# Kernel tuning notes

Measured on AMD Instinct MI355X. Metric: run time of the kernel, lower is better.

Reference implementation:

```python
import jax, jax.numpy as jnp
import numpy as np

N_NODES = 100000


def gcn_conv(x, edge_src, edge_dst, edge_weight, W, b):
    # support = x @ W ; out = A @ support + b  (A given as weighted edge list)
    h = x @ W                                   # [N, d_out]
    msg = h[edge_src] * edge_weight[:, None]     # [E, d_out]
    agg = jax.ops.segment_sum(msg, edge_dst, num_segments=N_NODES)
    return agg + b


def setup_inputs() -> dict:
    key = jax.random.key(0)
    ks = jax.random.split(key, 8)
    N, E, m, hidden, m_y = N_NODES, 1600000, 128, 64, 32
    x = jax.random.normal(ks[0], (N, m), dtype=jnp.float32)
    edge_src = jax.random.randint(ks[1], (E,), 0, N, dtype=jnp.int32)
    edge_dst = jax.random.randint(ks[2], (E,), 0, N, dtype=jnp.int32)
    edge_weight = jax.random.uniform(ks[3], (E,), dtype=jnp.float32)
    s1 = 1.0 / np.sqrt(m)
    s2 = 1.0 / np.sqrt(hidden)
    W1 = jax.random.uniform(ks[4], (m, hidden), dtype=jnp.float32, minval=-s1, maxval=s1)
    b1 = jax.random.uniform(ks[5], (hidden,), dtype=jnp.float32, minval=-s1, maxval=s1)
    W2 = jax.random.uniform(ks[6], (hidden, m_y), dtype=jnp.float32, minval=-s2, maxval=s2)
    b2 = jax.random.uniform(ks[7], (m_y,), dtype=jnp.float32, minval=-s2, maxval=s2)
    return {"x": x, "edge_src": edge_src, "edge_dst": edge_dst,
            "edge_weight": edge_weight, "W1": W1, "b1": b1, "W2": W2, "b2": b2}


def reference(x, edge_src, edge_dst, edge_weight, W1, b1, W2, b2):
    out = gcn_conv(x, edge_src, edge_dst, edge_weight, W1, b1)
    out = jax.nn.relu(out)
    # F.dropout(p=0.5, training=self.training) -> identity in eval mode
    out = gcn_conv(out, edge_src, edge_dst, edge_weight, W2, b2)
    return out
```

## Files before the change

### kernel.cpp

```cpp
#include <hip/hip_runtime.h>
#include <hip/hip_bf16.h>


typedef unsigned short u16;
typedef unsigned int uint;
typedef short short8 __attribute__((ext_vector_type(8)));
typedef float floatx4 __attribute__((ext_vector_type(4)));

static __device__ __forceinline__ u16 f2bf(float f) {
    unsigned int u = __float_as_uint(f);
    return (u16)((u + 0x7fff + ((u >> 16) & 1)) >> 16);
}

#define F4C(v, j) ((j)==0?(v).x:((j)==1?(v).y:((j)==2?(v).z:(v).w)))
#define CHUNK 2048

__global__ __launch_bounds__(256) void init_kernel(
    const float* __restrict__ W1, u16* __restrict__ wfg, int* __restrict__ gcursor)
{
    const int idx = blockIdx.x * 256 + threadIdx.x;
    if (idx < 512) gcursor[idx] = 0;
    const float4 v = ((const float4*)W1)[idx];
    const int k = idx >> 4, n4 = (idx & 15) * 4;
    const int step = k >> 5, klane = (k >> 3) & 3, j = k & 7;
    #pragma unroll
    for (int c = 0; c < 4; c++) {
        int n = n4 + c;
        wfg[(((n >> 4) * 4 + step) * 64 + klane * 16 + (n & 15)) * 8 + j] = f2bf(F4C(v, c));
    }
}

union __align__(16) SharedU {
    struct {
        u16 xs[64][136];
        u16 wf[4][4][64][8];
    } g;
    struct {
        int2 stage[CHUNK];
        u16  stb[CHUNK];
        int  hist[512], sc[512], xscan[512], place[512], runbase[512];
    } p;
};

__global__ __launch_bounds__(256, 4) void g1p_kernel(
    const float* __restrict__ x, const u16* __restrict__ wfg,
    u16* __restrict__ h1, int N,
    const int* __restrict__ src, const int* __restrict__ dst,
    const float* __restrict__ w, int* __restrict__ gcursor,
    int2* __restrict__ es, int E, int cap, int pblocks)
{
    __shared__ SharedU sh;
    const int tid = threadIdx.x;

    if (blockIdx.x < pblocks) {
        const int base = blockIdx.x * CHUNK;
        const int nloc = min(CHUNK, E - base);

        sh.p.hist[tid] = 0; sh.p.hist[tid + 256] = 0;
        __syncthreads();
        for (int i = tid; i < nloc; i += 256)
            atomicAdd(&sh.p.hist[dst[base + i] >> 8], 1);
        __syncthreads();

        sh.p.sc[tid] = sh.p.hist[tid];
        sh.p.sc[tid + 256] = sh.p.hist[tid + 256];
        __syncthreads();
        for (int o = 1; o < 512; o <<= 1) {
            int v0 = (tid >= o) ? sh.p.sc[tid - o] : 0;
            int v1 = (tid + 256 >= o) ? sh.p.sc[tid + 256 - o] : 0;
            __syncthreads();
            sh.p.sc[tid] += v0;
            sh.p.sc[tid + 256] += v1;
            __syncthreads();
        }
        sh.p.xscan[tid] = sh.p.sc[tid] - sh.p.hist[tid];
        sh.p.xscan[tid + 256] = sh.p.sc[tid + 256] - sh.p.hist[tid + 256];
        sh.p.place[tid] = sh.p.xscan[tid];
        sh.p.place[tid + 256] = sh.p.xscan[tid + 256];
        __syncthreads();

        for (int i = tid; i < nloc; i += 256) {
            int d = dst[base + i];
            int b = d >> 8;
            int pos = atomicAdd(&sh.p.place[b], 1);
            sh.p.stage[pos] = make_int2(src[base + i] | ((d & 255) << 24),
                                        __float_as_int(w[base + i]));
            sh.p.stb[pos] = (u16)b;
        }
        __syncthreads();

        {
            int l0 = sh.p.hist[tid], l1 = sh.p.hist[tid + 256];
            sh.p.runbase[tid]       = l0 ? atomicAdd(&gcursor[tid], l0)       : 0;
            sh.p.runbase[tid + 256] = l1 ? atomicAdd(&gcursor[tid + 256], l1) : 0;
        }
        __syncthreads();

        for (int i = tid; i < nloc; i += 256) {
            int b = sh.p.stb[i];
            es[(size_t)b * cap + sh.p.runbase[b] + (i - sh.p.xscan[b])] = sh.p.stage[i];
        }
        return;
    }

    const int row0 = (blockIdx.x - pblocks) * 64;
    {
        const float4* wg4 = (const float4*)wfg;
        float4* wl4 = (float4*)&sh.g.wf[0][0][0][0];
        #pragma unroll
        for (int i = 0; i < 4; i++) wl4[tid + i*256] = wg4[tid + i*256];
    }
    {
        const float4* x4 = (const float4*)x;
        #pragma unroll
        for (int i = 0; i < 8; i++) {
            int idx = tid + i*256;
            int r = idx >> 5, kc = idx & 31;
            int gr = row0 + r;
            float4 v = make_float4(0.f,0.f,0.f,0.f);
            if (gr < N) v = x4[gr*32 + kc];
            ushort4 o;
            o.x = f2bf(v.x); o.y = f2bf(v.y); o.z = f2bf(v.z); o.w = f2bf(v.w);
            *(ushort4*)&sh.g.xs[r][kc*4] = o;
        }
    }
    __syncthreads();

    const int wave = tid >> 6, lane = tid & 63;
    const int m = lane & 15, quad = lane >> 4;
    const int rw = wave * 16;

    floatx4 acc[4] = {(floatx4)(0.f), (floatx4)(0.f), (floatx4)(0.f), (floatx4)(0.f)};
    #pragma unroll
    for (int step = 0; step < 4; step++) {
        short8 a = *(const short8*)&sh.g.xs[rw + m][step*32 + quad*8];
        #pragma unroll
        for (int nt = 0; nt < 4; nt++) {
            short8 b = *(const short8*)&sh.g.wf[nt][step][lane][0];
            acc[nt] = __builtin_amdgcn_mfma_f32_16x16x32_bf16(a, b, acc[nt], 0, 0, 0);
        }
    }
    #pragma unroll
    for (int nt = 0; nt < 4; nt++) {
        #pragma unroll
        for (int r = 0; r < 4; r++) {
            int gr = row0 + rw + quad*4 + r;
            if (gr < N) h1[(size_t)gr*64 + nt*16 + m] = f2bf(acc[nt][r]);
        }
    }
}

#define SCAP 6144
__global__ __launch_bounds__(512, 3) void sort2_kernel(
    const int2* __restrict__ es, const int* __restrict__ gcursor,
    int2* __restrict__ es2, int2* __restrict__ off2, int N, int cap, int nb)
{
    __shared__ int2 stage[SCAP];
    __shared__ int hist[256], sc[256], cur[256];
    const int t = threadIdx.x;
    const int b = blockIdx.x;
    const int e0 = b * cap;
    const int len = gcursor[b];
    const int nstage = min(len, SCAP);

    if (t < 256) hist[t] = 0;
    __syncthreads();
    for (int i = t; i < nstage; i += 512) {
        int2 e = es[e0 + i];
        stage[i] = e;
        atomicAdd(&hist[((unsigned)e.x) >> 24], 1);
    }
    for (int i = SCAP + t; i < len; i += 512)
        atomicAdd(&hist[((unsigned)es[e0 + i].x) >> 24], 1);
    __syncthreads();

    int v = 0;
    if (t < 256) { v = hist[t]; sc[t] = v; }
    __syncthreads();
    for (int o = 1; o < 256; o <<= 1) {
        int add = 0;
        if (t < 256 && t >= o) add = sc[t - o];
        __syncthreads();
        if (t < 256) sc[t] += add;
        __syncthreads();
    }
    if (t < 256) {
        int ex = sc[t] - v;
        cur[t] = ex;
        int g = b * 256 + t;
        if (g < N) off2[g] = make_int2(e0 + ex, e0 + ex + v);
    }
    __syncthreads();

    for (int i = t; i < nstage; i += 512) {
        int2 e = stage[i];
        int pos = e0 + atomicAdd(&cur[((unsigned)e.x) >> 24], 1);
        es2[pos] = e;
    }
    for (int i = SCAP + t; i < len; i += 512) {
        int2 e = es[e0 + i];
        int pos = e0 + atomicAdd(&cur[((unsigned)e.x) >> 24], 1);
        es2[pos] = e;
    }
}

__global__ __launch_bounds__(256, 8) void gather1_kernel(
    const u16* __restrict__ h1, const int2* __restrict__ es,
    const int2* __restrict__ off2, const float* __restrict__ b1,
    const float* __restrict__ W2, u16* __restrict__ h2, int N)
{
    __shared__ __align__(16) u16 ts[64][72];
    __shared__ __align__(16) u16 wf2[2][2][64][8];
    __shared__ float b1s[64];
    const int tid = threadIdx.x;

    {
        const float4* s4 = (const float4*)W2;
        #pragma unroll
        for (int i = 0; i < 2; i++) {
            int idx = tid + i*256;
            float4 v = s4[idx];
            int k = idx >> 3, n4 = (idx & 7) * 4;
            int step = k >> 5, quad = (k >> 3) & 3, j = k & 7;
            #pragma unroll
            for (int c = 0; c < 4; c++) {
                int n = n4 + c;
                wf2[n >> 4][step][quad*16 + (n & 15)][j] = f2bf(F4C(v, c));
            }
        }
        if (tid < 16) ((float4*)b1s)[tid] = ((const float4*)b1)[tid];
    }
    __syncthreads();

    const int wave = tid >> 6, lane = tid & 63;
    const int h = lane >> 4, fl = lane & 15;
    const int node0 = blockIdx.x * 64 + wave * 16;
    const uint2* h1v = (const uint2*)h1;
    uint* tsu = (uint*)&ts[0][0];

    const int2 sg = off2[min(node0 + fl, N - 1)];

    #pragma unroll 1
    for (int i = 0; i < 16; i++) {
        const int pbeg = __builtin_amdgcn_readlane(sg.x, i);
        const int pend = __builtin_amdgcn_readlane(sg.y, i);
        const int cl = pend - 1;
        float a0 = 0.f, a1 = 0.f, a2 = 0.f, a3 = 0.f;
        #pragma unroll 1
        for (int p = pbeg; p < pend; p += 16) {
            const int i0 = p + h, i1 = p + 4 + h, i2 = p + 8 + h, i3 = p + 12 + h;
            int2 e0 = es[min(i0, cl)];
            int2 e1 = es[min(i1, cl)];
            int2 e2 = es[min(i2, cl)];
            int2 e3 = es[min(i3, cl)];
            uint2 v0 = h1v[(size_t)(e0.x & 0xFFFFFF) * 16 + fl];
            uint2 v1 = h1v[(size_t)(e1.x & 0xFFFFFF) * 16 + fl];
            uint2 v2 = h1v[(size_t)(e2.x & 0xFFFFFF) * 16 + fl];
            uint2 v3 = h1v[(size_t)(e3.x & 0xFFFFFF) * 16 + fl];
            float w0 = (i0 < pend) ? __int_as_float(e0.y) : 0.f;
            float w1 = (i1 < pend) ? __int_as_float(e1.y) : 0.f;
            float w2 = (i2 < pend) ? __int_as_float(e2.y) : 0.f;
            float w3 = (i3 < pend) ? __int_as_float(e3.y) : 0.f;
            a0 += __uint_as_float(v0.x << 16) * w0 + __uint_as_float(v1.x << 16) * w1
                + __uint_as_float(v2.x << 16) * w2 + __uint_as_float(v3.x << 16) * w3;
            a1 += __uint_as_float(v0.x & 0xFFFF0000u) * w0 + __uint_as_float(v1.x & 0xFFFF0000u) * w1
                + __uint_as_float(v2.x & 0xFFFF0000u) * w2 + __uint_as_float(v3.x & 0xFFFF0000u) * w3;
            a2 += __uint_as_float(v0.y << 16) * w0 + __uint_as_float(v1.y << 16) * w1
                + __uint_as_float(v2.y << 16) * w2 + __uint_as_float(v3.y << 16) * w3;
            a3 += __uint_as_float(v0.y & 0xFFFF0000u) * w0 + __uint_as_float(v1.y & 0xFFFF0000u) * w1
                + __uint_as_float(v2.y & 0xFFFF0000u) * w2 + __uint_as_float(v3.y & 0xFFFF0000u) * w3;
        }
        a0 += __shfl_xor(a0, 16, 64); a1 += __shfl_xor(a1, 16, 64);
        a2 += __shfl_xor(a2, 16, 64); a3 += __shfl_xor(a3, 16, 64);
        a0 += __shfl_xor(a0, 32, 64); a1 += __shfl_xor(a1, 32, 64);
        a2 += __shfl_xor(a2, 32, 64); a3 += __shfl_xor(a3, 32, 64);
        if (h == 0) {
            uint t0 = (uint)f2bf(fmaxf(a0 + b1s[4*fl],     0.f))
                    | ((uint)f2bf(fmaxf(a1 + b1s[4*fl + 1], 0.f)) << 16);
            uint t1 = (uint)f2bf(fmaxf(a2 + b1s[4*fl + 2], 0.f))
                    | ((uint)f2bf(fmaxf(a3 + b1s[4*fl + 3], 0.f)) << 16);
            *(uint2*)&tsu[(wave*16 + i) * 36 + 2*fl] = make_uint2(t0, t1);
        }
    }

    const int m = lane & 15, quad = lane >> 4;
    floatx4 acc[2] = {(floatx4)(0.f), (floatx4)(0.f)};
    #pragma unroll
    for (int step = 0; step < 2; step++) {
        short8 a = *(const short8*)&ts[wave*16 + m][step*32 + quad*8];
        #pragma unroll
        for (int nt = 0; nt < 2; nt++) {
            short8 b = *(const short8*)&wf2[nt][step][lane][0];
            acc[nt] = __builtin_amdgcn_mfma_f32_16x16x32_bf16(a, b, acc[nt], 0, 0, 0);
        }
    }
    #pragma unroll
    for (int nt = 0; nt < 2; nt++) {
        #pragma unroll
        for (int r = 0; r < 4; r++) {
            int g = node0 + quad*4 + r;
            if (g < N) h2[(size_t)g*32 + nt*16 + m] = f2bf(acc[nt][r]);
        }
    }
}

__global__ __launch_bounds__(256, 8) void gather2_kernel(
    const u16* __restrict__ h2, const int2* __restrict__ es,
    const int2* __restrict__ off2, const float* __restrict__ b2,
    float* __restrict__ out, int N)
{
    const int tid = threadIdx.x;
    const int wave = tid >> 6, lane = tid & 63;
    const int g = lane >> 3, fl = lane & 7;
    const int node0 = blockIdx.x * 64 + wave * 16;
    const uint2* h2v = (const uint2*)h2;

    const int2 sg = off2[min(node0 + (lane & 15), N - 1)];
    const float4 bb = ((const float4*)b2)[fl];

    #pragma unroll 1
    for (int i = 0; i < 16; i++) {
        const int pbeg = __builtin_amdgcn_readlane(sg.x, i);
        const int pend = __builtin_amdgcn_readlane(sg.y, i);
        const int cl = pend - 1;
        float a0 = 0.f, a1 = 0.f, a2 = 0.f, a3 = 0.f;
        #pragma unroll 1
        for (int p = pbeg; p < pend; p += 32) {
            const int i0 = p + g, i1 = p + 8 + g, i2 = p + 16 + g, i3 = p + 24 + g;
            int2 e0 = es[min(i0, cl)];
            int2 e1 = es[min(i1, cl)];
            int2 e2 = es[min(i2, cl)];
            int2 e3 = es[min(i3, cl)];
            uint2 v0 = h2v[(size_t)(e0.x & 0xFFFFFF) * 8 + fl];
            uint2 v1 = h2v[(size_t)(e1.x & 0xFFFFFF) * 8 + fl];
            uint2 v2 = h2v[(size_t)(e2.x & 0xFFFFFF) * 8 + fl];
            uint2 v3 = h2v[(size_t)(e3.x & 0xFFFFFF) * 8 + fl];
            float w0 = (i0 < pend) ? __int_as_float(e0.y) : 0.f;
            float w1 = (i1 < pend) ? __int_as_float(e1.y) : 0.f;
            float w2 = (i2 < pend) ? __int_as_float(e2.y) : 0.f;
            float w3 = (i3 < pend) ? __int_as_float(e3.y) : 0.f;
            a0 += __uint_as_float(v0.x << 16) * w0 + __uint_as_float(v1.x << 16) * w1
                + __uint_as_float(v2.x << 16) * w2 + __uint_as_float(v3.x << 16) * w3;
            a1 += __uint_as_float(v0.x & 0xFFFF0000u) * w0 + __uint_as_float(v1.x & 0xFFFF0000u) * w1
                + __uint_as_float(v2.x & 0xFFFF0000u) * w2 + __uint_as_float(v3.x & 0xFFFF0000u) * w3;
            a2 += __uint_as_float(v0.y << 16) * w0 + __uint_as_float(v1.y << 16) * w1
                + __uint_as_float(v2.y << 16) * w2 + __uint_as_float(v3.y << 16) * w3;
            a3 += __uint_as_float(v0.y & 0xFFFF0000u) * w0 + __uint_as_float(v1.y & 0xFFFF0000u) * w1
                + __uint_as_float(v2.y & 0xFFFF0000u) * w2 + __uint_as_float(v3.y & 0xFFFF0000u) * w3;
        }
        a0 += __shfl_xor(a0, 8, 64);  a1 += __shfl_xor(a1, 8, 64);
        a2 += __shfl_xor(a2, 8, 64);  a3 += __shfl_xor(a3, 8, 64);
        a0 += __shfl_xor(a0, 16, 64); a1 += __shfl_xor(a1, 16, 64);
        a2 += __shfl_xor(a2, 16, 64); a3 += __shfl_xor(a3, 16, 64);
        a0 += __shfl_xor(a0, 32, 64); a1 += __shfl_xor(a1, 32, 64);
        a2 += __shfl_xor(a2, 32, 64); a3 += __shfl_xor(a3, 32, 64);
        const int d = node0 + i;
        if (g == 0 && d < N)
            *(float4*)&out[(size_t)d * 32 + 4 * fl] =
                make_float4(a0 + bb.x, a1 + bb.y, a2 + bb.z, a3 + bb.w);
    }
}

extern "C" void kernel_launch(void* const* d_in, const int* in_sizes, int n_in,
                              void* d_out, int out_size, void* d_ws, size_t ws_size,
                              hipStream_t stream)
{
    const float* x   = (const float*)d_in[0];
    const int*  esrc = (const int*)d_in[1];
    const int*  edst = (const int*)d_in[2];
    const float* ew  = (const float*)d_in[3];
    const float* W1  = (const float*)d_in[4];
    const float* b1  = (const float*)d_in[5];
    const float* W2  = (const float*)d_in[6];
    const float* b2  = (const float*)d_in[7];
    float* out = (float*)d_out;

    const int N = in_sizes[0] / 128;
    const int E = in_sizes[1];
    const int nb = (N + 255) >> 8;

    const int mean = (E + nb - 1) / nb;
    int s = 1; while (s * s < mean) s++;
    const int cap = (mean + 8 * s + 15) & ~15;

    char* base = (char*)d_ws;
    size_t o = 0;
    auto alloc = [&](size_t bytes) { char* p = base + o; o = (o + bytes + 255) & ~(size_t)255; return p; };
    u16*  h1      = (u16*) alloc((size_t)N * 64 * 2);
    u16*  h2      = (u16*) alloc((size_t)N * 32 * 2);
    int2* es      = (int2*)alloc((size_t)nb * cap * 8);
    int2* es2     = (int2*)alloc((size_t)nb * cap * 8);
    int2* off2    = (int2*)alloc((size_t)N * 8);
    int*  gcursor = (int*) alloc(512 * 4);
    u16*  wfg     = (u16*) alloc(8192 * 2);

    const int pblocks = (E + CHUNK - 1) / CHUNK;
    const int gblocks = (N + 63) / 64;

    init_kernel<<<8, 256, 0, stream>>>(W1, wfg, gcursor);
    g1p_kernel<<<pblocks + gblocks, 256, 0, stream>>>(
        x, wfg, h1, N, esrc, edst, ew, gcursor, es, E, cap, pblocks);
    sort2_kernel<<<nb, 512, 0, stream>>>(es, gcursor, es2, off2, N, cap, nb);
    gather1_kernel<<<(N + 63) / 64, 256, 0, stream>>>(h1, es2, off2, b1, W2, h2, N);
    gather2_kernel<<<(N + 63) / 64, 256, 0, stream>>>(h2, es2, off2, b2, out, N);
}
```

Baseline: 237.7 us.

## Stage per-wave edge lists in LDS and interleave two nodes per gather loop

Each wave first copies the contiguous edge range of its 16 destination nodes (up to 384 edges) from global memory into shared memory with coalesced loads. The inner loops then read edges from LDS and process two nodes (j and j+8) at once, which doubles the independent feature gathers in flight and amortises the variable-degree loop overhead. Waves whose range exceeds the capacity fall back to the old path. The occupancy hint in launch bounds drops from 8 to 4, which gives more registers and LDS per block but may reduce latency hiding. Iterations of the paired loop run for the longer of the two degrees, so some lanes do masked, wasted work.

After: 221.1 us. -6.9%, faster.

```diff
diff --git a/kernel.cpp b/kernel.cpp
--- a/kernel.cpp
+++ b/kernel.cpp
@@ -14,6 +14,7 @@
 
 #define F4C(v, j) ((j)==0?(v).x:((j)==1?(v).y:((j)==2?(v).z:(v).w)))
 #define CHUNK 2048
+#define ECAP 384
 
 __global__ __launch_bounds__(256) void init_kernel(
     const float* __restrict__ W1, u16* __restrict__ wfg, int* __restrict__ gcursor)
@@ -204,7 +205,7 @@
     }
 }
 
-__global__ __launch_bounds__(256, 8) void gather1_kernel(
+__global__ __launch_bounds__(256, 4) void gather1_kernel(
     const u16* __restrict__ h1, const int2* __restrict__ es,
     const int2* __restrict__ off2, const float* __restrict__ b1,
     const float* __restrict__ W2, u16* __restrict__ h2, int N)
@@ -212,6 +213,7 @@
     __shared__ __align__(16) u16 ts[64][72];
     __shared__ __align__(16) u16 wf2[2][2][64][8];
     __shared__ float b1s[64];
+    __shared__ int2 eb[4][ECAP];
     const int tid = threadIdx.x;
 
     {
@@ -239,47 +241,134 @@
     uint* tsu = (uint*)&ts[0][0];
 
     const int2 sg = off2[min(node0 + fl, N - 1)];
-
-    #pragma unroll 1
-    for (int i = 0; i < 16; i++) {
-        const int pbeg = __builtin_amdgcn_readlane(sg.x, i);
-        const int pend = __builtin_amdgcn_readlane(sg.y, i);
-        const int cl = pend - 1;
-        float a0 = 0.f, a1 = 0.f, a2 = 0.f, a3 = 0.f;
+    const int beg = __builtin_amdgcn_readfirstlane(sg.x);
+    const int end = __builtin_amdgcn_readlane(sg.y, 15);
+    const int len = end - beg;
+
+    if (len <= ECAP) {
+        for (int k = lane; k < len; k += 64) eb[wave][k] = es[beg + k];
+
         #pragma unroll 1
-        for (int p = pbeg; p < pend; p += 16) {
-            const int i0 = p + h, i1 = p + 4 + h, i2 = p + 8 + h, i3 = p + 12 + h;
-            int2 e0 = es[min(i0, cl)];
-            int2 e1 = es[min(i1, cl)];
-            int2 e2 = es[min(i2, cl)];
-            int2 e3 = es[min(i3, cl)];
-            uint2 v0 = h1v[(size_t)(e0.x & 0xFFFFFF) * 16 + fl];
-            uint2 v1 = h1v[(size_t)(e1.x & 0xFFFFFF) * 16 + fl];
-            uint2 v2 = h1v[(size_t)(e2.x & 0xFFFFFF) * 16 + fl];
-            uint2 v3 = h1v[(size_t)(e3.x & 0xFFFFFF) * 16 + fl];
-            float w0 = (i0 < pend) ? __int_as_float(e0.y) : 0.f;
-            float w1 = (i1 < pend) ? __int_as_float(e1.y) : 0.f;
-            float w2 = (i2 < pend) ? __int_as_float(e2.y) : 0.f;
-            float w3 = (i3 < pend) ? __int_as_float(e3.y) : 0.f;
-            a0 += __uint_as_float(v0.x << 16) * w0 + __uint_as_float(v1.x << 16) * w1
-                + __uint_as_float(v2.x << 16) * w2 + __uint_as_float(v3.x << 16) * w3;
-            a1 += __uint_as_float(v0.x & 0xFFFF0000u) * w0 + __uint_as_float(v1.x & 0xFFFF0000u) * w1
-                + __uint_as_float(v2.x & 0xFFFF0000u) * w2 + __uint_as_float(v3.x & 0xFFFF0000u) * w3;
-            a2 += __uint_as_float(v0.y << 16) * w0 + __uint_as_float(v1.y << 16) * w1
-                + __uint_as_float(v2.y << 16) * w2 + __uint_as_float(v3.y << 16) * w3;
-            a3 += __uint_as_float(v0.y & 0xFFFF0000u) * w0 + __uint_as_float(v1.y & 0xFFFF0000u) * w1
-                + __uint_as_float(v2.y & 0xFFFF0000u) * w2 + __uint_as_float(v3.y & 0xFFFF0000u) * w3;
-        }
-        a0 += __shfl_xor(a0, 16, 64); a1 += __shfl_xor(a1, 16, 64);
-        a2 += __shfl_xor(a2, 16, 64); a3 += __shfl_xor(a3, 16, 64);
-        a0 += __shfl_xor(a0, 32, 64); a1 += __shfl_xor(a1, 32, 64);
-        a2 += __shfl_xor(a2, 32, 64); a3 += __shfl_xor(a3, 32, 64);
-        if (h == 0) {
-            uint t0 = (uint)f2bf(fmaxf(a0 + b1s[4*fl],     0.f))
-                    | ((uint)f2bf(fmaxf(a1 + b1s[4*fl + 1], 0.f)) << 16);
-            uint t1 = (uint)f2bf(fmaxf(a2 + b1s[4*fl + 2], 0.f))
-                    | ((uint)f2bf(fmaxf(a3 + b1s[4*fl + 3], 0.f)) << 16);
-            *(uint2*)&tsu[(wave*16 + i) * 36 + 2*fl] = make_uint2(t0, t1);
+        for (int j = 0; j < 8; j++) {
+            const int pbegA = __builtin_amdgcn_readlane(sg.x, j) - beg;
+            const int pendA = __builtin_amdgcn_readlane(sg.y, j) - beg;
+            const int pbegB = __builtin_amdgcn_readlane(sg.x, j + 8) - beg;
+            const int pendB = __builtin_amdgcn_readlane(sg.y, j + 8) - beg;
+            const int clA = max(pendA - 1, 0), clB = max(pendB - 1, 0);
+            float a0 = 0.f, a1 = 0.f, a2 = 0.f, a3 = 0.f;
+            float c0 = 0.f, c1 = 0.f, c2 = 0.f, c3 = 0.f;
+            int pA = pbegA, pB = pbegB;
+            #pragma unroll 1
+            while (pA < pendA || pB < pendB) {
+                const int iA0 = pA + h,     iA1 = pA + 4 + h;
+                const int iA2 = pA + 8 + h, iA3 = pA + 12 + h;
+                const int iB0 = pB + h,     iB1 = pB + 4 + h;
+                const int iB2 = pB + 8 + h, iB3 = pB + 12 + h;
+                int2 eA0 = eb[wave][min(iA0, clA)];
+                int2 eA1 = eb[wave][min(iA1, clA)];
+                int2 eA2 = eb[wave][min(iA2, clA)];
+                int2 eA3 = eb[wave][min(iA3, clA)];
+                int2 eB0 = eb[wave][min(iB0, clB)];
+                int2 eB1 = eb[wave][min(iB1, clB)];
+                int2 eB2 = eb[wave][min(iB2, clB)];
+                int2 eB3 = eb[wave][min(iB3, clB)];
+                uint2 vA0 = h1v[(size_t)(eA0.x & 0xFFFFFF) * 16 + fl];
+                uint2 vA1 = h1v[(size_t)(eA1.x & 0xFFFFFF) * 16 + fl];
+                uint2 vA2 = h1v[(size_t)(eA2.x & 0xFFFFFF) * 16 + fl];
+                uint2 vA3 = h1v[(size_t)(eA3.x & 0xFFFFFF) * 16 + fl];
+                uint2 vB0 = h1v[(size_t)(eB0.x & 0xFFFFFF) * 16 + fl];
+                uint2 vB1 = h1v[(size_t)(eB1.x & 0xFFFFFF) * 16 + fl];
+                uint2 vB2 = h1v[(size_t)(eB2.x & 0xFFFFFF) * 16 + fl];
+                uint2 vB3 = h1v[(size_t)(eB3.x & 0xFFFFFF) * 16 + fl];
+                float wA0 = (iA0 < pendA) ? __int_as_float(eA0.y) : 0.f;
+                float wA1 = (iA1 < pendA) ? __int_as_float(eA1.y) : 0.f;
+                float wA2 = (iA2 < pendA) ? __int_as_float(eA2.y) : 0.f;
+                float wA3 = (iA3 < pendA) ? __int_as_float(eA3.y) : 0.f;
+                float wB0 = (iB0 < pendB) ? __int_as_float(eB0.y) : 0.f;
+                float wB1 = (iB1 < pendB) ? __int_as_float(eB1.y) : 0.f;
+                float wB2 = (iB2 < pendB) ? __int_as_float(eB2.y) : 0.f;
+                float wB3 = (iB3 < pendB) ? __int_as_float(eB3.y) : 0.f;
+                a0 += __uint_as_float(vA0.x << 16) * wA0 + __uint_as_float(vA1.x << 16) * wA1
+                    + __uint_as_float(vA2.x << 16) * wA2 + __uint_as_float(vA3.x << 16) * wA3;
+                a1 += __uint_as_float(vA0.x & 0xFFFF0000u) * wA0 + __uint_as_float(vA1.x & 0xFFFF0000u) * wA1
+                    + __uint_as_float(vA2.x & 0xFFFF0000u) * wA2 + __uint_as_float(vA3.x & 0xFFFF0000u) * wA3;
+                a2 += __uint_as_float(vA0.y << 16) * wA0 + __uint_as_float(vA1.y << 16) * wA1
+                    + __uint_as_float(vA2.y << 16) * wA2 + __uint_as_float(vA3.y << 16) * wA3;
+                a3 += __uint_as_float(vA0.y & 0xFFFF0000u) * wA0 + __uint_as_float(vA1.y & 0xFFFF0000u) * wA1
+                    + __uint_as_float(vA2.y & 0xFFFF0000u) * wA2 + __uint_as_float(vA3.y & 0xFFFF0000u) * wA3;
+                c0 += __uint_as_float(vB0.x << 16) * wB0 + __uint_as_float(vB1.x << 16) * wB1
+                    + __uint_as_float(vB2.x << 16) * wB2 + __uint_as_float(vB3.x << 16) * wB3;
+                c1 += __uint_as_float(vB0.x & 0xFFFF0000u) * wB0 + __uint_as_float(vB1.x & 0xFFFF0000u) * wB1
+                    + __uint_as_float(vB2.x & 0xFFFF0000u) * wB2 + __uint_as_float(vB3.x & 0xFFFF0000u) * wB3;
+                c2 += __uint_as_float(vB0.y << 16) * wB0 + __uint_as_float(vB1.y << 16) * wB1
+                    + __uint_as_float(vB2.y << 16) * wB2 + __uint_as_float(vB3.y << 16) * wB3;
+                c3 += __uint_as_float(vB0.y & 0xFFFF0000u) * wB0 + __uint_as_float(vB1.y & 0xFFFF0000u) * wB1
+                    + __uint_as_float(vB2.y & 0xFFFF0000u) * wB2 + __uint_as_float(vB3.y & 0xFFFF0000u) * wB3;
+                pA += 16; pB += 16;
+            }
+            a0 += __shfl_xor(a0, 16, 64); a1 += __shfl_xor(a1, 16, 64);
+            a2 += __shfl_xor(a2, 16, 64); a3 += __shfl_xor(a3, 16, 64);
+            a0 += __shfl_xor(a0, 32, 64); a1 += __shfl_xor(a1, 32, 64);
+            a2 += __shfl_xor(a2, 32, 64); a3 += __shfl_xor(a3, 32, 64);
+            c0 += __shfl_xor(c0, 16, 64); c1 += __shfl_xor(c1, 16, 64);
+            c2 += __shfl_xor(c2, 16, 64); c3 += __shfl_xor(c3, 16, 64);
+            c0 += __shfl_xor(c0, 32, 64); c1 += __shfl_xor(c1, 32, 64);
+            c2 += __shfl_xor(c2, 32, 64); c3 += __shfl_xor(c3, 32, 64);
+            if (h == 0) {
+                uint t0 = (uint)f2bf(fmaxf(a0 + b1s[4*fl],     0.f))
+                        | ((uint)f2bf(fmaxf(a1 + b1s[4*fl + 1], 0.f)) << 16);
+                uint t1 = (uint)f2bf(fmaxf(a2 + b1s[4*fl + 2], 0.f))
+                        | ((uint)f2bf(fmaxf(a3 + b1s[4*fl + 3], 0.f)) << 16);
+                *(uint2*)&tsu[(wave*16 + j) * 36 + 2*fl] = make_uint2(t0, t1);
+                uint t2 = (uint)f2bf(fmaxf(c0 + b1s[4*fl],     0.f))
+                        | ((uint)f2bf(fmaxf(c1 + b1s[4*fl + 1], 0.f)) << 16);
+                uint t3 = (uint)f2bf(fmaxf(c2 + b1s[4*fl + 2], 0.f))
+                        | ((uint)f2bf(fmaxf(c3 + b1s[4*fl + 3], 0.f)) << 16);
+                *(uint2*)&tsu[(wave*16 + j + 8) * 36 + 2*fl] = make_uint2(t2, t3);
+            }
+        }
+    } else {
+        #pragma unroll 1
+        for (int i = 0; i < 16; i++) {
+            const int pbeg = __builtin_amdgcn_readlane(sg.x, i);
+            const int pend = __builtin_amdgcn_readlane(sg.y, i);
+            const int cl = max(pend - 1, 0);
+            float a0 = 0.f, a1 = 0.f, a2 = 0.f, a3 = 0.f;
+            #pragma unroll 1
+            for (int p = pbeg; p < pend; p += 16) {
+                const int i0 = p + h, i1 = p + 4 + h, i2 = p + 8 + h, i3 = p + 12 + h;
+                int2 e0 = es[min(i0, cl)];
+                int2 e1 = es[min(i1, cl)];
+                int2 e2 = es[min(i2, cl)];
+                int2 e3 = es[min(i3, cl)];
+                uint2 v0 = h1v[(size_t)(e0.x & 0xFFFFFF) * 16 + fl];
+                uint2 v1 = h1v[(size_t)(e1.x & 0xFFFFFF) * 16 + fl];
+                uint2 v2 = h1v[(size_t)(e2.x & 0xFFFFFF) * 16 + fl];
+                uint2 v3 = h1v[(size_t)(e3.x & 0xFFFFFF) * 16 + fl];
+                float w0 = (i0 < pend) ? __int_as_float(e0.y) : 0.f;
+                float w1 = (i1 < pend) ? __int_as_float(e1.y) : 0.f;
+                float w2 = (i2 < pend) ? __int_as_float(e2.y) : 0.f;
+                float w3 = (i3 < pend) ? __int_as_float(e3.y) : 0.f;
+                a0 += __uint_as_float(v0.x << 16) * w0 + __uint_as_float(v1.x << 16) * w1
+                    + __uint_as_float(v2.x << 16) * w2 + __uint_as_float(v3.x << 16) * w3;
+                a1 += __uint_as_float(v0.x & 0xFFFF0000u) * w0 + __uint_as_float(v1.x & 0xFFFF0000u) * w1
+                    + __uint_as_float(v2.x & 0xFFFF0000u) * w2 + __uint_as_float(v3.x & 0xFFFF0000u) * w3;
+                a2 += __uint_as_float(v0.y << 16) * w0 + __uint_as_float(v1.y << 16) * w1
+                    + __uint_as_float(v2.y << 16) * w2 + __uint_as_float(v3.y << 16) * w3;
+                a3 += __uint_as_float(v0.y & 0xFFFF0000u) * w0 + __uint_as_float(v1.y & 0xFFFF0000u) * w1
+                    + __uint_as_float(v2.y & 0xFFFF0000u) * w2 + __uint_as_float(v3.y & 0xFFFF0000u) * w3;
+            }
+            a0 += __shfl_xor(a0, 16, 64); a1 += __shfl_xor(a1, 16, 64);
+            a2 += __shfl_xor(a2, 16, 64); a3 += __shfl_xor(a3, 16, 64);
+            a0 += __shfl_xor(a0, 32, 64); a1 += __shfl_xor(a1, 32, 64);
+            a2 += __shfl_xor(a2, 32, 64); a3 += __shfl_xor(a3, 32, 64);
+            if (h == 0) {
+                uint t0 = (uint)f2bf(fmaxf(a0 + b1s[4*fl],     0.f))
+                        | ((uint)f2bf(fmaxf(a1 + b1s[4*fl + 1], 0.f)) << 16);
+                uint t1 = (uint)f2bf(fmaxf(a2 + b1s[4*fl + 2], 0.f))
+                        | ((uint)f2bf(fmaxf(a3 + b1s[4*fl + 3], 0.f)) << 16);
+                *(uint2*)&tsu[(wave*16 + i) * 36 + 2*fl] = make_uint2(t0, t1);
+            }
         }
     }
 
@@ -304,11 +393,12 @@
     }
 }
 
-__global__ __launch_bounds__(256, 8) void gather2_kernel(
+__global__ __launch_bounds__(256, 4) void gather2_kernel(
     const u16* __restrict__ h2, const int2* __restrict__ es,
     const int2* __restrict__ off2, const float* __restrict__ b2,
     float* __restrict__ out, int N)
 {
+    __shared__ int2 eb[4][ECAP];
     const int tid = threadIdx.x;
     const int wave = tid >> 6, lane = tid & 63;
     const int g = lane >> 3, fl = lane & 7;
@@ -316,48 +406,112 @@
     const uint2* h2v = (const uint2*)h2;
 
     const int2 sg = off2[min(node0 + (lane & 15), N - 1)];
+    const int beg = __builtin_amdgcn_readfirstlane(sg.x);
+    const int end = __builtin_amdgcn_readlane(sg.y, 15);
+    const int len = end - beg;
     const float4 bb = ((const float4*)b2)[fl];
 
-    #pragma unroll 1
-    for (int i = 0; i < 16; i++) {
-        const int pbeg = __builtin_amdgcn_readlane(sg.x, i);
-        const int pend = __builtin_amdgcn_readlane(sg.y, i);
-        const int cl = pend - 1;
-        float a0 = 0.f, a1 = 0.f, a2 = 0.f, a3 = 0.f;
+    if (len <= ECAP) {
+        for (int k = lane; k < len; k += 64) eb[wave][k] = es[beg + k];
+
         #pragma unroll 1
-        for (int p = pbeg; p < pend; p += 32) {
-            const int i0 = p + g, i1 = p + 8 + g, i2 = p + 16 + g, i3 = p + 24 + g;
-            int2 e0 = es[min(i0, cl)];
-            int2 e1 = es[min(i1, cl)];
-            int2 e2 = es[min(i2, cl)];
-            int2 e3 = es[min(i3, cl)];
-            uint2 v0 = h2v[(size_t)(e0.x & 0xFFFFFF) * 8 + fl];
-            uint2 v1 = h2v[(size_t)(e1.x & 0xFFFFFF) * 8 + fl];
-            uint2 v2 = h2v[(size_t)(e2.x & 0xFFFFFF) * 8 + fl];
-            uint2 v3 = h2v[(size_t)(e3.x & 0xFFFFFF) * 8 + fl];
-            float w0 = (i0 < pend) ? __int_as_float(e0.y) : 0.f;
-            float w1 = (i1 < pend) ? __int_as_float(e1.y) : 0.f;
-            float w2 = (i2 < pend) ? __int_as_float(e2.y) : 0.f;
-            float w3 = (i3 < pend) ? __int_as_float(e3.y) : 0.f;
-            a0 += __uint_as_float(v0.x << 16) * w0 + __uint_as_float(v1.x << 16) * w1
-                + __uint_as_float(v2.x << 16) * w2 + __uint_as_float(v3.x << 16) * w3;
-            a1 += __uint_as_float(v0.x & 0xFFFF0000u) * w0 + __uint_as_float(v1.x & 0xFFFF0000u) * w1
-                + __uint_as_float(v2.x & 0xFFFF0000u) * w2 + __uint_as_float(v3.x & 0xFFFF0000u) * w3;
-            a2 += __uint_as_float(v0.y << 16) * w0 + __uint_as_float(v1.y << 16) * w1
-                + __uint_as_float(v2.y << 16) * w2 + __uint_as_float(v3.y << 16) * w3;
-            a3 += __uint_as_float(v0.y & 0xFFFF0000u) * w0 + __uint_as_float(v1.y & 0xFFFF0000u) * w1
-                + __uint_as_float(v2.y & 0xFFFF0000u) * w2 + __uint_as_float(v3.y & 0xFFFF0000u) * w3;
-        }
-        a0 += __shfl_xor(a0, 8, 64);  a1 += __shfl_xor(a1, 8, 64);
-        a2 += __shfl_xor(a2, 8, 64);  a3 += __shfl_xor(a3, 8, 64);
-        a0 += __shfl_xor(a0, 16, 64); a1 += __shfl_xor(a1, 16, 64);
-        a2 += __shfl_xor(a2, 16, 64); a3 += __shfl_xor(a3, 16, 64);
-        a0 += __shfl_xor(a0, 32, 64); a1 += __shfl_xor(a1, 32, 64);
-        a2 += __shfl_xor(a2, 32, 64); a3 += __shfl_xor(a3, 32, 64);
-        const int d = node0 + i;
-        if (g == 0 && d < N)
-            *(float4*)&out[(size_t)d * 32 + 4 * fl] =
-                make_float4(a0 + bb.x, a1 + bb.y, a2 + bb.z, a3 + bb.w);
+        for (int j = 0; j < 8; j++) {
+            const int pbegA = __builtin_amdgcn_readlane(sg.x, j) - beg;
+            const int pendA = __builtin_amdgcn_readlane(sg.y, j) - beg;
+            const int pbegB = __builtin_amdgcn_readlane(sg.x, j + 8) - beg;
+            const int pendB = __builtin_amdgcn_readlane(sg.y, j + 8) - beg;
+            const int clA = max(pendA - 1, 0), clB = max(pendB - 1, 0);
+            float a0 = 0.f, a1 = 0.f, a2 = 0.f, a3 = 0.f;
+            float c0 = 0.f, c1 = 0.f, c2 = 0.f, c3 = 0.f;
+            int pA = pbegA, pB = pbegB;
+            #pragma unroll 1
+            while (pA < pendA || pB < pendB) {
+                const int iA0 = pA + g, iA1 = pA + 8 + g;
+                const int iB0 = pB + g, iB1 = pB + 8 + g;
+                int2 eA0 = eb[wave][min(iA0, clA)];
+                int2 eA1 = eb[wave][min(iA1, clA)];
+                int2 eB0 = eb[wave][min(iB0, clB)];
+                int2 eB1 = eb[wave][min(iB1, clB)];
+                uint2 vA0 = h2v[(size_t)(eA0.x & 0xFFFFFF) * 8 + fl];
+                uint2 vA1 = h2v[(size_t)(eA1.x & 0xFFFFFF) * 8 + fl];
+                uint2 vB0 = h2v[(size_t)(eB0.x & 0xFFFFFF) * 8 + fl];
+                uint2 vB1 = h2v[(size_t)(eB1.x & 0xFFFFFF) * 8 + fl];
+                float wA0 = (iA0 < pendA) ? __int_as_float(eA0.y) : 0.f;
+                float wA1 = (iA1 < pendA) ? __int_as_float(eA1.y) : 0.f;
+                float wB0 = (iB0 < pendB) ? __int_as_float(eB0.y) : 0.f;
+                float wB1 = (iB1 < pendB) ? __int_as_float(eB1.y) : 0.f;
+                a0 += __uint_as_float(vA0.x << 16) * wA0 + __uint_as_float(vA1.x << 16) * wA1;
+                a1 += __uint_as_float(vA0.x & 0xFFFF0000u) * wA0 + __uint_as_float(vA1.x & 0xFFFF0000u) * wA1;
+                a2 += __uint_as_float(vA0.y << 16) * wA0 + __uint_as_float(vA1.y << 16) * wA1;
+                a3 += __uint_as_float(vA0.y & 0xFFFF0000u) * wA0 + __uint_as_float(vA1.y & 0xFFFF0000u) * wA1;
+                c0 += __uint_as_float(vB0.x << 16) * wB0 + __uint_as_float(vB1.x << 16) * wB1;
+                c1 += __uint_as_float(vB0.x & 0xFFFF0000u) * wB0 + __uint_as_float(vB1.x & 0xFFFF0000u) * wB1;
+                c2 += __uint_as_float(vB0.y << 16) * wB0 + __uint_as_float(vB1.y << 16) * wB1;
+                c3 += __uint_as_float(vB0.y & 0xFFFF0000u) * wB0 + __uint_as_float(vB1.y & 0xFFFF0000u) * wB1;
+                pA += 16; pB += 16;
+            }
+            a0 += __shfl_xor(a0, 8, 64);  a1 += __shfl_xor(a1, 8, 64);
+            a2 += __shfl_xor(a2, 8, 64);  a3 += __shfl_xor(a3, 8, 64);
+            a0 += __shfl_xor(a0, 16, 64); a1 += __shfl_xor(a1, 16, 64);
+            a2 += __shfl_xor(a2, 16, 64); a3 += __shfl_xor(a3, 16, 64);
+            a0 += __shfl_xor(a0, 32, 64); a1 += __shfl_xor(a1, 32, 64);
+            a2 += __shfl_xor(a2, 32, 64); a3 += __shfl_xor(a3, 32, 64);
+            c0 += __shfl_xor(c0, 8, 64);  c1 += __shfl_xor(c1, 8, 64);
+            c2 += __shfl_xor(c2, 8, 64);  c3 += __shfl_xor(c3, 8, 64);
+            c0 += __shfl_xor(c0, 16, 64); c1 += __shfl_xor(c1, 16, 64);
+            c2 += __shfl_xor(c2, 16, 64); c3 += __shfl_xor(c3, 16, 64);
+            c0 += __shfl_xor(c0, 32, 64); c1 += __shfl_xor(c1, 32, 64);
+            c2 += __shfl_xor(c2, 32, 64); c3 += __shfl_xor(c3, 32, 64);
+            const int dA = node0 + j, dB = node0 + j + 8;
+            if (g == 0 && dA < N)
+                *(float4*)&out[(size_t)dA * 32 + 4 * fl] =
+                    make_float4(a0 + bb.x, a1 + bb.y, a2 + bb.z, a3 + bb.w);
+            if (g == 0 && dB < N)
+                *(float4*)&out[(size_t)dB * 32 + 4 * fl] =
+                    make_float4(c0 + bb.x, c1 + bb.y, c2 + bb.z, c3 + bb.w);
+        }
+    } else {
+        #pragma unroll 1
+        for (int i = 0; i < 16; i++) {
+            const int pbeg = __builtin_amdgcn_readlane(sg.x, i);
+            const int pend = __builtin_amdgcn_readlane(sg.y, i);
+            const int cl = max(pend - 1, 0);
+            float a0 = 0.f, a1 = 0.f, a2 = 0.f, a3 = 0.f;
+            #pragma unroll 1
+            for (int p = pbeg; p < pend; p += 32) {
+                const int i0 = p + g, i1 = p + 8 + g, i2 = p + 16 + g, i3 = p + 24 + g;
+                int2 e0 = es[min(i0, cl)];
+                int2 e1 = es[min(i1, cl)];
+                int2 e2 = es[min(i2, cl)];
+                int2 e3 = es[min(i3, cl)];
+                uint2 v0 = h2v[(size_t)(e0.x & 0xFFFFFF) * 8 + fl];
+                uint2 v1 = h2v[(size_t)(e1.x & 0xFFFFFF) * 8 + fl];
+                uint2 v2 = h2v[(size_t)(e2.x & 0xFFFFFF) * 8 + fl];
+                uint2 v3 = h2v[(size_t)(e3.x & 0xFFFFFF) * 8 + fl];
+                float w0 = (i0 < pend) ? __int_as_float(e0.y) : 0.f;
+                float w1 = (i1 < pend) ? __int_as_float(e1.y) : 0.f;
+                float w2 = (i2 < pend) ? __int_as_float(e2.y) : 0.f;
+                float w3 = (i3 < pend) ? __int_as_float(e3.y) : 0.f;
+                a0 += __uint_as_float(v0.x << 16) * w0 + __uint_as_float(v1.x << 16) * w1
+                    + __uint_as_float(v2.x << 16) * w2 + __uint_as_float(v3.x << 16) * w3;
+                a1 += __uint_as_float(v0.x & 0xFFFF0000u) * w0 + __uint_as_float(v1.x & 0xFFFF0000u) * w1
+                    + __uint_as_float(v2.x & 0xFFFF0000u) * w2 + __uint_as_float(v3.x & 0xFFFF0000u) * w3;
+                a2 += __uint_as_float(v0.y << 16) * w0 + __uint_as_float(v1.y << 16) * w1
+                    + __uint_as_float(v2.y << 16) * w2 + __uint_as_float(v3.y << 16) * w3;
+                a3 += __uint_as_float(v0.y & 0xFFFF0000u) * w0 + __uint_as_float(v1.y & 0xFFFF0000u) * w1
+                    + __uint_as_float(v2.y & 0xFFFF0000u) * w2 + __uint_as_float(v3.y & 0xFFFF0000u) * w3;
+            }
+            a0 += __shfl_xor(a0, 8, 64);  a1 += __shfl_xor(a1, 8, 64);
+            a2 += __shfl_xor(a2, 8, 64);  a3 += __shfl_xor(a3, 8, 64);
+            a0 += __shfl_xor(a0, 16, 64); a1 += __shfl_xor(a1, 16, 64);
+            a2 += __shfl_xor(a2, 16, 64); a3 += __shfl_xor(a3, 16, 64);
+            a0 += __shfl_xor(a0, 32, 64); a1 += __shfl_xor(a1, 32, 64);
+            a2 += __shfl_xor(a2, 32, 64); a3 += __shfl_xor(a3, 32, 64);
+            const int d = node0 + i;
+            if (g == 0 && d < N)
+                *(float4*)&out[(size_t)d * 32 + 4 * fl] =
+                    make_float4(a0 + bb.x, a1 + bb.y, a2 + bb.z, a3 + bb.w);
+        }
     }
 }
 
```
